# Kernel optimization log

Hardware: AMD Instinct MI355X
Metric: run time of the kernel (lower is better)

The kernel has to match this reference:

```python
import jax, jax.numpy as jnp
import numpy as np

EPS = 1e-5

def sage_layer(x, src, dst, n_tgt, Wl, bl, Wr, gamma, beta):
    # mean aggregation of source features over incoming edges per target
    msg = x[src]                                         # [E, C] irregular gather
    s = jax.ops.segment_sum(msg, dst, num_segments=n_tgt)
    cnt = jax.ops.segment_sum(jnp.ones((src.shape[0],), x.dtype), dst, num_segments=n_tgt)
    aggr = s / jnp.maximum(cnt, 1.0)[:, None]
    x_tgt = x[:n_tgt]
    h = aggr @ Wl.T + bl + x_tgt @ Wr.T                  # SAGEConv: lin_l(aggr)+lin_r(root)
    h = jax.nn.relu(h)
    mu = jnp.mean(h, axis=0)
    var = jnp.mean((h - mu) ** 2, axis=0)                # biased var (torch BN training)
    return gamma * (h - mu) * jax.lax.rsqrt(var + EPS) + beta

def setup_inputs() -> dict:
    key = jax.random.key(0)
    ks = jax.random.split(key, 16)
    C = 256
    N0, N1, N2 = 200000, 50000, 12500
    E0, E1 = 800000, 400000
    sc = 1.0 / np.sqrt(C)
    return {
        "x": jax.random.normal(ks[0], (N0, C), jnp.float32),
        "ei0_src": jax.random.randint(ks[1], (E0,), 0, N0),
        "ei0_dst": jax.random.randint(ks[2], (E0,), 0, N1),
        "ei1_src": jax.random.randint(ks[3], (E1,), 0, N1),
        "ei1_dst": jax.random.randint(ks[4], (E1,), 0, N2),
        "Wl0": jax.random.normal(ks[5], (C, C), jnp.float32) * sc,
        "bl0": jnp.zeros((C,), jnp.float32),
        "Wr0": jax.random.normal(ks[6], (C, C), jnp.float32) * sc,
        "g0": jnp.ones((C,), jnp.float32),
        "be0": jnp.zeros((C,), jnp.float32),
        "Wl1": jax.random.normal(ks[7], (C, C), jnp.float32) * sc,
        "bl1": jnp.zeros((C,), jnp.float32),
        "Wr1": jax.random.normal(ks[8], (C, C), jnp.float32) * sc,
        "g1": jnp.ones((C,), jnp.float32),
        "be1": jnp.zeros((C,), jnp.float32),
    }

def reference(x, ei0_src, ei0_dst, ei1_src, ei1_dst,
              Wl0, bl0, Wr0, g0, be0, Wl1, bl1, Wr1, g1, be1):
    N1, N2 = 50000, 12500
    x = sage_layer(x, ei0_src, ei0_dst, N1, Wl0, bl0, Wr0, g0, be0)
    x = sage_layer(x, ei1_src, ei1_dst, N2, Wl1, bl1, Wr1, g1, be1)
    return x
```

## Files before the change

kernel.cpp:

```cpp
#include <hip/hip_runtime.h>
#include <cstddef>
#include <cstdint>

#define C 256

typedef __attribute__((ext_vector_type(8))) short short8;
typedef __attribute__((ext_vector_type(4))) float f32x4;

__device__ __forceinline__ ushort f2bf(float f) {
    uint32_t u = __float_as_uint(f);
    u += 0x7FFF + ((u >> 16) & 1);
    return (ushort)(u >> 16);
}
__device__ __forceinline__ float bf2f(ushort u) {
    return __uint_as_float(((uint32_t)u) << 16);
}
__device__ __forceinline__ uint2 pack4(float a, float b, float c, float d) {
    uint2 o;
    o.x = (uint32_t)f2bf(a) | ((uint32_t)f2bf(b) << 16);
    o.y = (uint32_t)f2bf(c) | ((uint32_t)f2bf(d) << 16);
    return o;
}
__device__ __forceinline__ void acc8(uint4 v, float* a) {
    a[0] += bf2f((ushort)(v.x & 0xffff)); a[1] += bf2f((ushort)(v.x >> 16));
    a[2] += bf2f((ushort)(v.y & 0xffff)); a[3] += bf2f((ushort)(v.y >> 16));
    a[4] += bf2f((ushort)(v.z & 0xffff)); a[5] += bf2f((ushort)(v.z >> 16));
    a[6] += bf2f((ushort)(v.w & 0xffff)); a[7] += bf2f((ushort)(v.w >> 16));
}

__global__ __launch_bounds__(256) void cast_kernel(
        const float4* __restrict__ x4, int nx4, uint2* __restrict__ xbf,
        const float4* __restrict__ wl0f, const float4* __restrict__ wr0f,
        uint2* __restrict__ wl0b, uint2* __restrict__ wr0b) {
    const int nw4 = C * C / 4;
    const int total = nx4 + 2 * nw4;
    const int stride = gridDim.x * blockDim.x;
    for (int i = blockIdx.x * blockDim.x + threadIdx.x; i < total; i += stride) {
        if (i < nx4) {
            float4 v = x4[i];
            xbf[i] = pack4(v.x, v.y, v.z, v.w);
        } else if (i < nx4 + nw4) {
            int j = i - nx4;
            float4 v = wl0f[j];
            wl0b[j] = pack4(v.x, v.y, v.z, v.w);
        } else {
            int j = i - nx4 - nw4;
            float4 v = wr0f[j];
            wr0b[j] = pack4(v.x, v.y, v.z, v.w);
        }
    }
}

#define HB0 2048
#define HB1 1024
__global__ __launch_bounds__(256) void hist_kernel(
        const int* __restrict__ e0d, int* __restrict__ cnt0, int E0,
        const int* __restrict__ e1d, int* __restrict__ cnt1, int E1) {
    const int b = blockIdx.x;
    if (b < HB0) {
        const int stride = HB0 * 256;
        for (int i = b * 256 + threadIdx.x; i < E0; i += stride)
            atomicAdd(&cnt0[e0d[i]], 1);
    } else {
        const int stride = HB1 * 256;
        for (int i = (b - HB0) * 256 + threadIdx.x; i < E1; i += stride)
            atomicAdd(&cnt1[e1d[i]], 1);
    }
}

__global__ __launch_bounds__(1024) void scan2_kernel(
        const int* __restrict__ cnt0, int* __restrict__ off0, int n0,
        const int* __restrict__ cnt1, int* __restrict__ off1, int n1) {
    const int* cnt = blockIdx.x ? cnt1 : cnt0;
    int* off = blockIdx.x ? off1 : off0;
    int n = blockIdx.x ? n1 : n0;
    __shared__ int buf[1024];
    int chunk = (n + 1023) >> 10;
    int lo = (int)threadIdx.x * chunk;
    int hi = min(lo + chunk, n);
    int s = 0;
    for (int i = lo; i < hi; ++i) s += cnt[i];
    buf[threadIdx.x] = s;
    __syncthreads();
    int xv = s;
    for (int d = 1; d < 1024; d <<= 1) {
        int t = ((int)threadIdx.x >= d) ? buf[threadIdx.x - d] : 0;
        __syncthreads();
        xv += t;
        buf[threadIdx.x] = xv;
        __syncthreads();
    }
    int run = xv - s;
    for (int i = lo; i < hi; ++i) { off[i] = run; run += cnt[i]; }
    if (lo < n && hi == n) off[n] = run;
}

__global__ void scatter2_kernel(
        const int* __restrict__ s0, const int* __restrict__ d0,
        const int* __restrict__ off0, int* __restrict__ cnt0, int* __restrict__ esrc0, int E0,
        const int* __restrict__ s1, const int* __restrict__ d1,
        const int* __restrict__ off1, int* __restrict__ cnt1, int* __restrict__ esrc1, int E1) {
    int e = blockIdx.x * blockDim.x + threadIdx.x;
    if (e < E0) {
        int d = d0[e];
        int old = atomicSub(&cnt0[d], 1);
        esrc0[off0[d] + old - 1] = s0[e];
    } else if (e < E0 + E1) {
        int i = e - E0;
        int d = d1[i];
        int old = atomicSub(&cnt1[d], 1);
        esrc1[off1[d] + old - 1] = s1[i];
    }
}

__global__ __launch_bounds__(256) void aggregate_kernel(const uint4* __restrict__ xb4,
        const int* __restrict__ esrc, const int* __restrict__ off,
        uint4* __restrict__ out4, int n_tgt) {
    const int lane = threadIdx.x & 63;
    const int half = lane >> 5, l31 = lane & 31;
    const int t = blockIdx.x * 4 + (threadIdx.x >> 6);
    if (t >= n_tgt) return;
    const int base = off[t];
    const int deg = off[t + 1] - base;
    float a[8] = {0.f, 0.f, 0.f, 0.f, 0.f, 0.f, 0.f, 0.f};
    int i = 0;
    for (; i + 8 <= deg; i += 8) {
        int s0 = esrc[base + i + half];
        int s1 = esrc[base + i + 2 + half];
        int s2 = esrc[base + i + 4 + half];
        int s3 = esrc[base + i + 6 + half];
        uint4 v0 = xb4[(size_t)s0 * 32 + l31];
        uint4 v1 = xb4[(size_t)s1 * 32 + l31];
        uint4 v2 = xb4[(size_t)s2 * 32 + l31];
        uint4 v3 = xb4[(size_t)s3 * 32 + l31];
        acc8(v0, a); acc8(v1, a); acc8(v2, a); acc8(v3, a);
    }
    for (; i + 2 <= deg; i += 2) {
        int s = esrc[base + i + half];
        uint4 v = xb4[(size_t)s * 32 + l31];
        acc8(v, a);
    }
    if ((deg & 1) && half == 0) {
        int s = esrc[base + deg - 1];
        uint4 v = xb4[(size_t)s * 32 + l31];
        acc8(v, a);
    }
#pragma unroll
    for (int j = 0; j < 8; ++j) a[j] += __shfl_xor(a[j], 32, 64);
    if (half == 0) {
        float inv = 1.0f / (float)(deg > 1 ? deg : 1);
        uint4 o;
        o.x = (uint32_t)f2bf(a[0] * inv) | ((uint32_t)f2bf(a[1] * inv) << 16);
        o.y = (uint32_t)f2bf(a[2] * inv) | ((uint32_t)f2bf(a[3] * inv) << 16);
        o.z = (uint32_t)f2bf(a[4] * inv) | ((uint32_t)f2bf(a[5] * inv) << 16);
        o.w = (uint32_t)f2bf(a[6] * inv) | ((uint32_t)f2bf(a[7] * inv) << 16);
        out4[(size_t)t * 32 + l31] = o;
    }
}

__global__ __launch_bounds__(256) void aggregate_f32_kernel(const float4* __restrict__ x4,
        const int* __restrict__ esrc, const int* __restrict__ off,
        uint2* __restrict__ aggr, int n_tgt) {
    int w = threadIdx.x >> 6;
    int lane = threadIdx.x & 63;
    int t = blockIdx.x * 4 + w;
    if (t >= n_tgt) return;
    int base = off[t];
    int deg = off[t + 1] - base;
    float4 acc = make_float4(0.f, 0.f, 0.f, 0.f);
    for (int i = 0; i < deg; ++i) {
        int s = esrc[base + i];
        float4 v = x4[(size_t)s * 64 + lane];
        acc.x += v.x; acc.y += v.y; acc.z += v.z; acc.w += v.w;
    }
    float inv = 1.0f / (float)(deg > 1 ? deg : 1);
    aggr[(size_t)t * 64 + lane] = pack4(acc.x * inv, acc.y * inv, acc.z * inv, acc.w * inv);
}

#define TM 128
#define TN 128
#define LDK 40

__global__ __launch_bounds__(256) void gemm_bn_mfma(
        const ushort* __restrict__ Aagg, const ushort* __restrict__ Axt,
        const ushort* __restrict__ Wl,  const ushort* __restrict__ Wr,
        const float* __restrict__ bias,
        ushort* __restrict__ h, float* __restrict__ colsum, float* __restrict__ colsq,
        int M) {
    __shared__ ushort As[TM * LDK];
    __shared__ ushort Bs[TN * LDK];
    __shared__ float csum[TN];
    __shared__ float csq[TN];

    const int tid = threadIdx.x;
    const int m0 = blockIdx.y * TM;
    const int n0 = blockIdx.x * TN;
    const int wid = tid >> 6, lane = tid & 63;
    const int l15 = lane & 15, quad = lane >> 4;
    const int wm = (wid & 1) * 64, wn = (wid >> 1) * 64;

    if (tid < TN) { csum[tid] = 0.f; csq[tid] = 0.f; }

    const int srow = tid >> 2;
    const int skoff = (tid & 3) * 8;

    f32x4 acc[4][4];
#pragma unroll
    for (int i = 0; i < 4; ++i)
#pragma unroll
        for (int j = 0; j < 4; ++j) acc[i][j] = (f32x4){0.f, 0.f, 0.f, 0.f};

#pragma unroll 1
    for (int kt = 0; kt < 16; ++kt) {
        const int ks = kt * 32;
        const ushort* Ab = (ks < 256) ? Aagg : Axt;
        const ushort* Bb = (ks < 256) ? Wl : Wr;
        const int k0 = ks & 255;
        int r0 = min(m0 + srow, M - 1);
        int r1 = min(m0 + srow + 64, M - 1);
        uint4 a0 = *(const uint4*)&Ab[(size_t)r0 * C + k0 + skoff];
        uint4 a1 = *(const uint4*)&Ab[(size_t)r1 * C + k0 + skoff];
        uint4 b0 = *(const uint4*)&Bb[(size_t)(n0 + srow) * C + k0 + skoff];
        uint4 b1 = *(const uint4*)&Bb[(size_t)(n0 + srow + 64) * C + k0 + skoff];
        __syncthreads();
        *(uint4*)&As[srow * LDK + skoff] = a0;
        *(uint4*)&As[(srow + 64) * LDK + skoff] = a1;
        *(uint4*)&Bs[srow * LDK + skoff] = b0;
        *(uint4*)&Bs[(srow + 64) * LDK + skoff] = b1;
        __syncthreads();

        short8 af[4], bw[4];
#pragma unroll
        for (int mi = 0; mi < 4; ++mi)
            af[mi] = *(const short8*)&As[(wm + mi * 16 + l15) * LDK + quad * 8];
#pragma unroll
        for (int ni = 0; ni < 4; ++ni)
            bw[ni] = *(const short8*)&Bs[(wn + ni * 16 + l15) * LDK + quad * 8];
#pragma unroll
        for (int mi = 0; mi < 4; ++mi)
#pragma unroll
            for (int ni = 0; ni < 4; ++ni)
                acc[mi][ni] = __builtin_amdgcn_mfma_f32_16x16x32_bf16(
                    af[mi], bw[ni], acc[mi][ni], 0, 0, 0);
    }

    float lsum[4] = {0.f, 0.f, 0.f, 0.f};
    float lsq[4]  = {0.f, 0.f, 0.f, 0.f};
#pragma unroll
    for (int ni = 0; ni < 4; ++ni) {
        const int col = wn + ni * 16 + l15;
        const float bv = bias[n0 + col];
#pragma unroll
        for (int mi = 0; mi < 4; ++mi) {
#pragma unroll
            for (int r = 0; r < 4; ++r) {
                int m = m0 + wm + mi * 16 + quad * 4 + r;
                float v = acc[mi][ni][r] + bv;
                v = fmaxf(v, 0.f);
                if (m < M) {
                    h[(size_t)m * C + n0 + col] = f2bf(v);
                    lsum[ni] += v;
                    lsq[ni] += v * v;
                }
            }
        }
    }
#pragma unroll
    for (int ni = 0; ni < 4; ++ni) {
        const int col = wn + ni * 16 + l15;
        atomicAdd(&csum[col], lsum[ni]);
        atomicAdd(&csq[col], lsq[ni]);
    }
    __syncthreads();
    if (tid < TN) {
        atomicAdd(&colsum[n0 + tid], csum[tid]);
        atomicAdd(&colsq[n0 + tid], csq[tid]);
    }
}

__global__ __launch_bounds__(256) void fixup_kernel(
        const float* __restrict__ colsum, const float* __restrict__ colsq, float invN,
        const float* __restrict__ g0, const float* __restrict__ be0,
        const float* __restrict__ Wl1, const float* __restrict__ Wr1,
        const float* __restrict__ bl1,
        ushort* __restrict__ wl1b, ushort* __restrict__ wr1b, float* __restrict__ bias1) {
    __shared__ float ss[C], st[C];
    __shared__ float red[256];
    const int k = threadIdx.x;
    {
        float m = colsum[k] * invN;
        float v = colsq[k] * invN - m * m;
        float r = rsqrtf(fmaxf(v, 0.f) + 1e-5f);
        float s = g0[k] * r;
        ss[k] = s;
        st[k] = be0[k] - m * s;
    }
    __syncthreads();
    const int n = blockIdx.x;
    float wl = Wl1[(size_t)n * C + k];
    float wr = Wr1[(size_t)n * C + k];
    wl1b[(size_t)n * C + k] = f2bf(wl * ss[k]);
    wr1b[(size_t)n * C + k] = f2bf(wr * ss[k]);
    red[k] = st[k] * (wl + wr);
    __syncthreads();
    for (int d = 128; d > 0; d >>= 1) {
        if (k < d) red[k] += red[k + d];
        __syncthreads();
    }
    if (k == 0) bias1[n] = bl1[n] + red[0];
}

__global__ __launch_bounds__(256) void norm1_kernel(const uint2* __restrict__ hin,
        const float* __restrict__ colsum, const float* __restrict__ colsq, float invN,
        const float* __restrict__ gamma, const float* __restrict__ beta,
        float4* __restrict__ outp, int n4) {
    __shared__ float smu[C], srs[C];
    {
        int k = threadIdx.x;
        float m = colsum[k] * invN;
        float v = colsq[k] * invN - m * m;
        smu[k] = m;
        srs[k] = rsqrtf(fmaxf(v, 0.f) + 1e-5f);
    }
    __syncthreads();
    int i = blockIdx.x * blockDim.x + threadIdx.x;
    if (i >= n4) return;
    int c = (i & 63) << 2;
    uint2 v = hin[i];
    float4 o;
    o.x = gamma[c + 0] * (bf2f((ushort)(v.x & 0xffff)) - smu[c + 0]) * srs[c + 0] + beta[c + 0];
    o.y = gamma[c + 1] * (bf2f((ushort)(v.x >> 16))    - smu[c + 1]) * srs[c + 1] + beta[c + 1];
    o.z = gamma[c + 2] * (bf2f((ushort)(v.y & 0xffff)) - smu[c + 2]) * srs[c + 2] + beta[c + 2];
    o.w = gamma[c + 3] * (bf2f((ushort)(v.y >> 16))    - smu[c + 3]) * srs[c + 3] + beta[c + 3];
    outp[i] = o;
}

extern "C" void kernel_launch(void* const* d_in, const int* in_sizes, int n_in,
                              void* d_out, int out_size, void* d_ws, size_t ws_size,
                              hipStream_t stream) {
    const float* x   = (const float*)d_in[0];
    const int* e0s   = (const int*)d_in[1];
    const int* e0d   = (const int*)d_in[2];
    const int* e1s   = (const int*)d_in[3];
    const int* e1d   = (const int*)d_in[4];
    const float* Wl0 = (const float*)d_in[5];
    const float* bl0 = (const float*)d_in[6];
    const float* Wr0 = (const float*)d_in[7];
    const float* ga0 = (const float*)d_in[8];
    const float* be0 = (const float*)d_in[9];
    const float* Wl1 = (const float*)d_in[10];
    const float* bl1 = (const float*)d_in[11];
    const float* Wr1 = (const float*)d_in[12];
    const float* ga1 = (const float*)d_in[13];
    const float* be1 = (const float*)d_in[14];

    const int N0 = 200000, N1 = 50000, N2 = 12500;
    const int E0 = in_sizes[1];
    const int E1 = in_sizes[3];

    char* ws = (char*)d_ws;
    size_t o = 0;
    auto alloc = [&](size_t bytes) -> char* {
        char* p = ws + o;
        o += (bytes + 255) & ~(size_t)255;
        return p;
    };

    const size_t common =
        (size_t)N1 * C * 2 * 2 + (size_t)E0 * 4 + (size_t)E1 * 4 +
        ((size_t)N1 + N2 + 8 * C) * 4 + ((size_t)N1 + N2 + 2) * 4 +
        4 * (size_t)C * C * 2 + C * 4 + 65536;
    const bool full = ws_size >= common + (size_t)N0 * C * 2;

    int* cnt0 = (int*)alloc(((size_t)N1 + N2 + 8 * C) * sizeof(int));
    int* cnt1 = cnt0 + N1;
    float* stats = (float*)(cnt1 + N2);
    float* colsum0 = stats,         *colsq0 = stats + C;
    float* colsum1 = stats + 4 * C, *colsq1 = stats + 5 * C;
    const size_t zbytes = ((size_t)N1 + N2 + 8 * C) * sizeof(int);

    int* off0 = (int*)alloc(((size_t)N1 + 1) * sizeof(int));
    int* off1 = (int*)alloc(((size_t)N2 + 1) * sizeof(int));
    ushort* x_bf  = (ushort*)alloc((full ? (size_t)N0 : (size_t)N1) * C * 2);
    ushort* aggr0 = (ushort*)alloc((size_t)N1 * C * 2);
    ushort* h0raw = (ushort*)alloc((size_t)N1 * C * 2);
    ushort* aggr1 = aggr0;
    ushort* h1raw = aggr0 + (size_t)N2 * C;
    int* esrc0 = (int*)alloc((size_t)E0 * sizeof(int));
    int* esrc1 = (int*)alloc((size_t)E1 * sizeof(int));
    ushort* wbf = (ushort*)alloc(4 * (size_t)C * C * 2);
    ushort* wl0b = wbf, *wr0b = wbf + C * C, *wl1b = wbf + 2 * C * C, *wr1b = wbf + 3 * C * C;
    float* bias1 = (float*)alloc(C * sizeof(float));

    hipMemsetAsync(cnt0, 0, zbytes, stream);

    {
        int nx4 = (full ? N0 : N1) * C / 4;
        cast_kernel<<<6400, 256, 0, stream>>>((const float4*)x, nx4, (uint2*)x_bf,
                                              (const float4*)Wl0, (const float4*)Wr0,
                                              (uint2*)wl0b, (uint2*)wr0b);
    }
    hist_kernel<<<HB0 + HB1, 256, 0, stream>>>(e0d, cnt0, E0, e1d, cnt1, E1);
    scan2_kernel<<<2, 1024, 0, stream>>>(cnt0, off0, N1, cnt1, off1, N2);
    scatter2_kernel<<<(E0 + E1 + 255) / 256, 256, 0, stream>>>(
        e0s, e0d, off0, cnt0, esrc0, E0, e1s, e1d, off1, cnt1, esrc1, E1);

    if (full)
        aggregate_kernel<<<N1 / 4, 256, 0, stream>>>((const uint4*)x_bf, esrc0, off0,
                                                     (uint4*)aggr0, N1);
    else
        aggregate_f32_kernel<<<N1 / 4, 256, 0, stream>>>((const float4*)x, esrc0, off0,
                                                         (uint2*)aggr0, N1);
    dim3 grid0(C / TN, (N1 + TM - 1) / TM);
    gemm_bn_mfma<<<grid0, 256, 0, stream>>>(aggr0, x_bf, wl0b, wr0b, bl0,
                                            h0raw, colsum0, colsq0, N1);
    fixup_kernel<<<C, 256, 0, stream>>>(colsum0, colsq0, 1.0f / (float)N1,
                                        ga0, be0, Wl1, Wr1, bl1, wl1b, wr1b, bias1);

    aggregate_kernel<<<N2 / 4, 256, 0, stream>>>((const uint4*)h0raw, esrc1, off1,
                                                 (uint4*)aggr1, N2);
    dim3 grid1(C / TN, (N2 + TM - 1) / TM);
    gemm_bn_mfma<<<grid1, 256, 0, stream>>>(aggr1, h0raw, wl1b, wr1b, bias1,
                                            h1raw, colsum1, colsq1, N2);
    int n4_1 = N2 * C / 4;
    norm1_kernel<<<(n4_1 + 255) / 256, 256, 0, stream>>>((const uint2*)h1raw,
                                                         colsum1, colsq1, 1.0f / (float)N2,
                                                         ga1, be1, (float4*)d_out, n4_1);
}
```

Baseline: 697.6 us.

## Fuse whole two-layer SAGE pipeline into one cooperative persistent megakernel

Replaces the chain of separate kernels (cast, histogram, scan, scatter, aggregate, gemm, fixup, norm) with one cooperative kernel that steps through the phases separated by grid.sync. The single-block scan is replaced by a multi-block two-level scan, and the phases use grid-stride or persistent tile loops. The aim is to remove launch gaps and the serial scan bottleneck. In exchange the grid is capped at 256–512 blocks, which limits parallelism in the gather and GEMM phases, and each of the many grid barriers adds its own cost. The f32 fallback path for small workspaces is also dropped.

```diff
diff --git a/kernel.cpp b/kernel.cpp
--- a/kernel.cpp
+++ b/kernel.cpp
@@ -1,8 +1,16 @@
 #include <hip/hip_runtime.h>
+#include <hip/hip_cooperative_groups.h>
 #include <cstddef>
 #include <cstdint>
 
+namespace cg = cooperative_groups;
+
 #define C 256
+#define N1_ 50000
+#define N2_ 12500
+#define TM 128
+#define TN 128
+#define LDK 40
 
 typedef __attribute__((ext_vector_type(8))) short short8;
 typedef __attribute__((ext_vector_type(4))) float f32x4;
@@ -28,181 +36,64 @@
     a[6] += bf2f((ushort)(v.w & 0xffff)); a[7] += bf2f((ushort)(v.w >> 16));
 }
 
-__global__ __launch_bounds__(256) void cast_kernel(
-        const float4* __restrict__ x4, int nx4, uint2* __restrict__ xbf,
-        const float4* __restrict__ wl0f, const float4* __restrict__ wr0f,
-        uint2* __restrict__ wl0b, uint2* __restrict__ wr0b) {
-    const int nw4 = C * C / 4;
-    const int total = nx4 + 2 * nw4;
-    const int stride = gridDim.x * blockDim.x;
-    for (int i = blockIdx.x * blockDim.x + threadIdx.x; i < total; i += stride) {
-        if (i < nx4) {
-            float4 v = x4[i];
-            xbf[i] = pack4(v.x, v.y, v.z, v.w);
-        } else if (i < nx4 + nw4) {
-            int j = i - nx4;
-            float4 v = wl0f[j];
-            wl0b[j] = pack4(v.x, v.y, v.z, v.w);
-        } else {
-            int j = i - nx4 - nw4;
-            float4 v = wr0f[j];
-            wr0b[j] = pack4(v.x, v.y, v.z, v.w);
-        }
-    }
-}
-
-#define HB0 2048
-#define HB1 1024
-__global__ __launch_bounds__(256) void hist_kernel(
-        const int* __restrict__ e0d, int* __restrict__ cnt0, int E0,
-        const int* __restrict__ e1d, int* __restrict__ cnt1, int E1) {
-    const int b = blockIdx.x;
-    if (b < HB0) {
-        const int stride = HB0 * 256;
-        for (int i = b * 256 + threadIdx.x; i < E0; i += stride)
-            atomicAdd(&cnt0[e0d[i]], 1);
-    } else {
-        const int stride = HB1 * 256;
-        for (int i = (b - HB0) * 256 + threadIdx.x; i < E1; i += stride)
-            atomicAdd(&cnt1[e1d[i]], 1);
-    }
-}
-
-__global__ __launch_bounds__(1024) void scan2_kernel(
-        const int* __restrict__ cnt0, int* __restrict__ off0, int n0,
-        const int* __restrict__ cnt1, int* __restrict__ off1, int n1) {
-    const int* cnt = blockIdx.x ? cnt1 : cnt0;
-    int* off = blockIdx.x ? off1 : off0;
-    int n = blockIdx.x ? n1 : n0;
-    __shared__ int buf[1024];
-    int chunk = (n + 1023) >> 10;
-    int lo = (int)threadIdx.x * chunk;
-    int hi = min(lo + chunk, n);
-    int s = 0;
-    for (int i = lo; i < hi; ++i) s += cnt[i];
-    buf[threadIdx.x] = s;
+struct MegaParams {
+    const float4* x4; int nx4;
+    uint2* xbf;
+    const float4* wl0f; const float4* wr0f;
+    uint2* wl0b2; uint2* wr0b2;
+    const int* e0s; const int* e0d; int E0;
+    const int* e1s; const int* e1d; int E1;
+    int* cnt0; int* cnt1;
+    int* off0; int* off1;
+    int* bsum0; int* bbase0; int* bsum1; int* bbase1;
+    int* esrc0; int* esrc1;
+    const ushort* xbf_u;
+    ushort* aggr0; ushort* h0raw; ushort* aggr1; ushort* h1raw;
+    const ushort* wl0b; const ushort* wr0b;
+    ushort* wl1b; ushort* wr1b;
+    const float* bl0; const float* ga0; const float* be0;
+    const float* Wl1f; const float* Wr1f; const float* bl1;
+    float* bias1;
+    const float* ga1; const float* be1;
+    float* colsum0; float* colsq0; float* colsum1; float* colsq1;
+    float4* out;
+};
+
+union alignas(16) Smem {
+    int scan[256];
+    struct { ushort As[TM * LDK]; ushort Bs[TN * LDK]; float csum[TN]; float csq[TN]; } g;
+    struct { float ss[C]; float st[C]; float red[256]; } fx;
+    struct { float mu[C]; float rs[C]; } nm;
+};
+
+__device__ __forceinline__ int block_incl_scan(int v, int* buf) {
+    const int t = threadIdx.x;
+    buf[t] = v;
     __syncthreads();
-    int xv = s;
-    for (int d = 1; d < 1024; d <<= 1) {
-        int t = ((int)threadIdx.x >= d) ? buf[threadIdx.x - d] : 0;
-        __syncthreads();
-        xv += t;
-        buf[threadIdx.x] = xv;
-        __syncthreads();
-    }
-    int run = xv - s;
-    for (int i = lo; i < hi; ++i) { off[i] = run; run += cnt[i]; }
-    if (lo < n && hi == n) off[n] = run;
-}
-
-__global__ void scatter2_kernel(
-        const int* __restrict__ s0, const int* __restrict__ d0,
-        const int* __restrict__ off0, int* __restrict__ cnt0, int* __restrict__ esrc0, int E0,
-        const int* __restrict__ s1, const int* __restrict__ d1,
-        const int* __restrict__ off1, int* __restrict__ cnt1, int* __restrict__ esrc1, int E1) {
-    int e = blockIdx.x * blockDim.x + threadIdx.x;
-    if (e < E0) {
-        int d = d0[e];
-        int old = atomicSub(&cnt0[d], 1);
-        esrc0[off0[d] + old - 1] = s0[e];
-    } else if (e < E0 + E1) {
-        int i = e - E0;
-        int d = d1[i];
-        int old = atomicSub(&cnt1[d], 1);
-        esrc1[off1[d] + old - 1] = s1[i];
-    }
-}
-
-__global__ __launch_bounds__(256) void aggregate_kernel(const uint4* __restrict__ xb4,
-        const int* __restrict__ esrc, const int* __restrict__ off,
-        uint4* __restrict__ out4, int n_tgt) {
-    const int lane = threadIdx.x & 63;
-    const int half = lane >> 5, l31 = lane & 31;
-    const int t = blockIdx.x * 4 + (threadIdx.x >> 6);
-    if (t >= n_tgt) return;
-    const int base = off[t];
-    const int deg = off[t + 1] - base;
-    float a[8] = {0.f, 0.f, 0.f, 0.f, 0.f, 0.f, 0.f, 0.f};
-    int i = 0;
-    for (; i + 8 <= deg; i += 8) {
-        int s0 = esrc[base + i + half];
-        int s1 = esrc[base + i + 2 + half];
-        int s2 = esrc[base + i + 4 + half];
-        int s3 = esrc[base + i + 6 + half];
-        uint4 v0 = xb4[(size_t)s0 * 32 + l31];
-        uint4 v1 = xb4[(size_t)s1 * 32 + l31];
-        uint4 v2 = xb4[(size_t)s2 * 32 + l31];
-        uint4 v3 = xb4[(size_t)s3 * 32 + l31];
-        acc8(v0, a); acc8(v1, a); acc8(v2, a); acc8(v3, a);
-    }
-    for (; i + 2 <= deg; i += 2) {
-        int s = esrc[base + i + half];
-        uint4 v = xb4[(size_t)s * 32 + l31];
-        acc8(v, a);
-    }
-    if ((deg & 1) && half == 0) {
-        int s = esrc[base + deg - 1];
-        uint4 v = xb4[(size_t)s * 32 + l31];
-        acc8(v, a);
-    }
-#pragma unroll
-    for (int j = 0; j < 8; ++j) a[j] += __shfl_xor(a[j], 32, 64);
-    if (half == 0) {
-        float inv = 1.0f / (float)(deg > 1 ? deg : 1);
-        uint4 o;
-        o.x = (uint32_t)f2bf(a[0] * inv) | ((uint32_t)f2bf(a[1] * inv) << 16);
-        o.y = (uint32_t)f2bf(a[2] * inv) | ((uint32_t)f2bf(a[3] * inv) << 16);
-        o.z = (uint32_t)f2bf(a[4] * inv) | ((uint32_t)f2bf(a[5] * inv) << 16);
-        o.w = (uint32_t)f2bf(a[6] * inv) | ((uint32_t)f2bf(a[7] * inv) << 16);
-        out4[(size_t)t * 32 + l31] = o;
-    }
-}
-
-__global__ __launch_bounds__(256) void aggregate_f32_kernel(const float4* __restrict__ x4,
-        const int* __restrict__ esrc, const int* __restrict__ off,
-        uint2* __restrict__ aggr, int n_tgt) {
-    int w = threadIdx.x >> 6;
-    int lane = threadIdx.x & 63;
-    int t = blockIdx.x * 4 + w;
-    if (t >= n_tgt) return;
-    int base = off[t];
-    int deg = off[t + 1] - base;
-    float4 acc = make_float4(0.f, 0.f, 0.f, 0.f);
-    for (int i = 0; i < deg; ++i) {
-        int s = esrc[base + i];
-        float4 v = x4[(size_t)s * 64 + lane];
-        acc.x += v.x; acc.y += v.y; acc.z += v.z; acc.w += v.w;
-    }
-    float inv = 1.0f / (float)(deg > 1 ? deg : 1);
-    aggr[(size_t)t * 64 + lane] = pack4(acc.x * inv, acc.y * inv, acc.z * inv, acc.w * inv);
-}
-
-#define TM 128
-#define TN 128
-#define LDK 40
-
-__global__ __launch_bounds__(256) void gemm_bn_mfma(
-        const ushort* __restrict__ Aagg, const ushort* __restrict__ Axt,
-        const ushort* __restrict__ Wl,  const ushort* __restrict__ Wr,
-        const float* __restrict__ bias,
-        ushort* __restrict__ h, float* __restrict__ colsum, float* __restrict__ colsq,
-        int M) {
-    __shared__ ushort As[TM * LDK];
-    __shared__ ushort Bs[TN * LDK];
-    __shared__ float csum[TN];
-    __shared__ float csq[TN];
-
+    for (int d = 1; d < 256; d <<= 1) {
+        int o = (t >= d) ? buf[t - d] : 0;
+        __syncthreads();
+        buf[t] += o;
+        __syncthreads();
+    }
+    return buf[t];
+}
+
+__device__ void gemm_tile(int tile, const ushort* __restrict__ Aagg, const ushort* __restrict__ Axt,
+                          const ushort* __restrict__ Wl, const ushort* __restrict__ Wr,
+                          const float* __restrict__ bias, ushort* __restrict__ h,
+                          float* __restrict__ colsum, float* __restrict__ colsq,
+                          int M, Smem& sm) {
     const int tid = threadIdx.x;
-    const int m0 = blockIdx.y * TM;
-    const int n0 = blockIdx.x * TN;
+    const int n0 = (tile & 1) * TN;
+    const int m0 = (tile >> 1) * TM;
     const int wid = tid >> 6, lane = tid & 63;
     const int l15 = lane & 15, quad = lane >> 4;
     const int wm = (wid & 1) * 64, wn = (wid >> 1) * 64;
-
-    if (tid < TN) { csum[tid] = 0.f; csq[tid] = 0.f; }
-
     const int srow = tid >> 2;
     const int skoff = (tid & 3) * 8;
+
+    if (tid < TN) { sm.g.csum[tid] = 0.f; sm.g.csq[tid] = 0.f; }
 
     f32x4 acc[4][4];
 #pragma unroll
@@ -223,19 +114,19 @@
         uint4 b0 = *(const uint4*)&Bb[(size_t)(n0 + srow) * C + k0 + skoff];
         uint4 b1 = *(const uint4*)&Bb[(size_t)(n0 + srow + 64) * C + k0 + skoff];
         __syncthreads();
-        *(uint4*)&As[srow * LDK + skoff] = a0;
-        *(uint4*)&As[(srow + 64) * LDK + skoff] = a1;
-        *(uint4*)&Bs[srow * LDK + skoff] = b0;
-        *(uint4*)&Bs[(srow + 64) * LDK + skoff] = b1;
+        *(uint4*)&sm.g.As[srow * LDK + skoff] = a0;
+        *(uint4*)&sm.g.As[(srow + 64) * LDK + skoff] = a1;
+        *(uint4*)&sm.g.Bs[srow * LDK + skoff] = b0;
+        *(uint4*)&sm.g.Bs[(srow + 64) * LDK + skoff] = b1;
         __syncthreads();
 
         short8 af[4], bw[4];
 #pragma unroll
         for (int mi = 0; mi < 4; ++mi)
-            af[mi] = *(const short8*)&As[(wm + mi * 16 + l15) * LDK + quad * 8];
+            af[mi] = *(const short8*)&sm.g.As[(wm + mi * 16 + l15) * LDK + quad * 8];
 #pragma unroll
         for (int ni = 0; ni < 4; ++ni)
-            bw[ni] = *(const short8*)&Bs[(wn + ni * 16 + l15) * LDK + quad * 8];
+            bw[ni] = *(const short8*)&sm.g.Bs[(wn + ni * 16 + l15) * LDK + quad * 8];
 #pragma unroll
         for (int mi = 0; mi < 4; ++mi)
 #pragma unroll
@@ -268,71 +159,217 @@
 #pragma unroll
     for (int ni = 0; ni < 4; ++ni) {
         const int col = wn + ni * 16 + l15;
-        atomicAdd(&csum[col], lsum[ni]);
-        atomicAdd(&csq[col], lsq[ni]);
+        atomicAdd(&sm.g.csum[col], lsum[ni]);
+        atomicAdd(&sm.g.csq[col], lsq[ni]);
     }
     __syncthreads();
     if (tid < TN) {
-        atomicAdd(&colsum[n0 + tid], csum[tid]);
-        atomicAdd(&colsq[n0 + tid], csq[tid]);
-    }
-}
-
-__global__ __launch_bounds__(256) void fixup_kernel(
-        const float* __restrict__ colsum, const float* __restrict__ colsq, float invN,
-        const float* __restrict__ g0, const float* __restrict__ be0,
-        const float* __restrict__ Wl1, const float* __restrict__ Wr1,
-        const float* __restrict__ bl1,
-        ushort* __restrict__ wl1b, ushort* __restrict__ wr1b, float* __restrict__ bias1) {
-    __shared__ float ss[C], st[C];
-    __shared__ float red[256];
-    const int k = threadIdx.x;
-    {
-        float m = colsum[k] * invN;
-        float v = colsq[k] * invN - m * m;
+        atomicAdd(&colsum[n0 + tid], sm.g.csum[tid]);
+        atomicAdd(&colsq[n0 + tid], sm.g.csq[tid]);
+    }
+}
+
+__device__ void aggregate_phase(const uint4* __restrict__ xb4, const int* __restrict__ esrc,
+                                const int* __restrict__ off, uint4* __restrict__ out4,
+                                int n_tgt, int nwaves) {
+    const int tid = threadIdx.x;
+    const int lane = tid & 63;
+    const int half = lane >> 5, l31 = lane & 31;
+    const int gw = blockIdx.x * 4 + (tid >> 6);
+    for (int t = gw; t < n_tgt; t += nwaves) {
+        const int base = off[t];
+        const int deg = off[t + 1] - base;
+        float a[8] = {0.f, 0.f, 0.f, 0.f, 0.f, 0.f, 0.f, 0.f};
+        int i = 0;
+        for (; i + 8 <= deg; i += 8) {
+            int s0 = esrc[base + i + half];
+            int s1 = esrc[base + i + 2 + half];
+            int s2 = esrc[base + i + 4 + half];
+            int s3 = esrc[base + i + 6 + half];
+            uint4 v0 = xb4[(size_t)s0 * 32 + l31];
+            uint4 v1 = xb4[(size_t)s1 * 32 + l31];
+            uint4 v2 = xb4[(size_t)s2 * 32 + l31];
+            uint4 v3 = xb4[(size_t)s3 * 32 + l31];
+            acc8(v0, a); acc8(v1, a); acc8(v2, a); acc8(v3, a);
+        }
+        for (; i + 2 <= deg; i += 2) {
+            int s = esrc[base + i + half];
+            uint4 v = xb4[(size_t)s * 32 + l31];
+            acc8(v, a);
+        }
+        if ((deg & 1) && half == 0) {
+            int s = esrc[base + deg - 1];
+            uint4 v = xb4[(size_t)s * 32 + l31];
+            acc8(v, a);
+        }
+#pragma unroll
+        for (int j = 0; j < 8; ++j) a[j] += __shfl_xor(a[j], 32, 64);
+        if (half == 0) {
+            float inv = 1.0f / (float)(deg > 1 ? deg : 1);
+            uint4 o;
+            o.x = (uint32_t)f2bf(a[0] * inv) | ((uint32_t)f2bf(a[1] * inv) << 16);
+            o.y = (uint32_t)f2bf(a[2] * inv) | ((uint32_t)f2bf(a[3] * inv) << 16);
+            o.z = (uint32_t)f2bf(a[4] * inv) | ((uint32_t)f2bf(a[5] * inv) << 16);
+            o.w = (uint32_t)f2bf(a[6] * inv) | ((uint32_t)f2bf(a[7] * inv) << 16);
+            out4[(size_t)t * 32 + l31] = o;
+        }
+    }
+}
+
+__global__ __launch_bounds__(256, 2) void mega_kernel(MegaParams p) {
+    cg::grid_group grid = cg::this_grid();
+    __shared__ Smem sm;
+    const int tid = threadIdx.x;
+    const int nblk = gridDim.x;
+    const int gtid = blockIdx.x * 256 + tid;
+    const int gsz = nblk * 256;
+    const int nwaves = nblk * 4;
+
+    {
+        const int nw4 = C * C / 4;
+        const int total = p.nx4 + 2 * nw4;
+        for (int i = gtid; i < total; i += gsz) {
+            if (i < p.nx4) {
+                float4 v = p.x4[i];
+                p.xbf[i] = pack4(v.x, v.y, v.z, v.w);
+            } else if (i < p.nx4 + nw4) {
+                int j = i - p.nx4;
+                float4 v = p.wl0f[j];
+                p.wl0b2[j] = pack4(v.x, v.y, v.z, v.w);
+            } else {
+                int j = i - p.nx4 - nw4;
+                float4 v = p.wr0f[j];
+                p.wr0b2[j] = pack4(v.x, v.y, v.z, v.w);
+            }
+        }
+        for (int i = gtid; i < p.E0; i += gsz) atomicAdd(&p.cnt0[p.e0d[i]], 1);
+        for (int i = gtid; i < p.E1; i += gsz) atomicAdd(&p.cnt1[p.e1d[i]], 1);
+    }
+    __threadfence(); grid.sync();
+
+    const int ch0 = (N1_ + nblk - 1) / nblk;
+    const int ch1 = (N2_ + nblk - 1) / nblk;
+    {
+        int i0 = blockIdx.x * ch0 + tid;
+        int v0 = (tid < ch0 && i0 < N1_) ? p.cnt0[i0] : 0;
+        int incl0 = block_incl_scan(v0, sm.scan);
+        if (tid == 255) p.bsum0[blockIdx.x] = incl0;
+        __syncthreads();
+        int i1 = blockIdx.x * ch1 + tid;
+        int v1 = (tid < ch1 && i1 < N2_) ? p.cnt1[i1] : 0;
+        int incl1 = block_incl_scan(v1, sm.scan);
+        if (tid == 255) p.bsum1[blockIdx.x] = incl1;
+    }
+    __threadfence(); grid.sync();
+
+    if (blockIdx.x < 2) {
+        const int* bs = blockIdx.x ? p.bsum1 : p.bsum0;
+        int* bb = blockIdx.x ? p.bbase1 : p.bbase0;
+        int a0 = (2 * tid < nblk) ? bs[2 * tid] : 0;
+        int a1 = (2 * tid + 1 < nblk) ? bs[2 * tid + 1] : 0;
+        int s = a0 + a1;
+        int incl = block_incl_scan(s, sm.scan);
+        int excl = incl - s;
+        if (2 * tid < nblk) bb[2 * tid] = excl;
+        if (2 * tid + 1 < nblk) bb[2 * tid + 1] = excl + a0;
+        if (tid == 255) {
+            if (blockIdx.x) p.off1[N2_] = incl;
+            else p.off0[N1_] = incl;
+        }
+    }
+    __threadfence(); grid.sync();
+
+    {
+        int i0 = blockIdx.x * ch0 + tid;
+        int v0 = (tid < ch0 && i0 < N1_) ? p.cnt0[i0] : 0;
+        int incl0 = block_incl_scan(v0, sm.scan);
+        if (tid < ch0 && i0 < N1_) p.off0[i0] = p.bbase0[blockIdx.x] + incl0 - v0;
+        __syncthreads();
+        int i1 = blockIdx.x * ch1 + tid;
+        int v1 = (tid < ch1 && i1 < N2_) ? p.cnt1[i1] : 0;
+        int incl1 = block_incl_scan(v1, sm.scan);
+        if (tid < ch1 && i1 < N2_) p.off1[i1] = p.bbase1[blockIdx.x] + incl1 - v1;
+    }
+    __threadfence(); grid.sync();
+
+    {
+        for (int e = gtid; e < p.E0; e += gsz) {
+            int d = p.e0d[e];
+            int old = atomicSub(&p.cnt0[d], 1);
+            p.esrc0[p.off0[d] + old - 1] = p.e0s[e];
+        }
+        for (int e = gtid; e < p.E1; e += gsz) {
+            int d = p.e1d[e];
+            int old = atomicSub(&p.cnt1[d], 1);
+            p.esrc1[p.off1[d] + old - 1] = p.e1s[e];
+        }
+    }
+    __threadfence(); grid.sync();
+
+    aggregate_phase((const uint4*)p.xbf_u, p.esrc0, p.off0, (uint4*)p.aggr0, N1_, nwaves);
+    __threadfence(); grid.sync();
+
+    {
+        const int ntiles = ((N1_ + TM - 1) / TM) * 2;
+        for (int t = blockIdx.x; t < ntiles; t += nblk)
+            gemm_tile(t, p.aggr0, p.xbf_u, p.wl0b, p.wr0b, p.bl0,
+                      p.h0raw, p.colsum0, p.colsq0, N1_, sm);
+    }
+    __threadfence(); grid.sync();
+
+    if (blockIdx.x < 256) {
+        const float invN = 1.0f / (float)N1_;
+        float m = p.colsum0[tid] * invN;
+        float v = p.colsq0[tid] * invN - m * m;
         float r = rsqrtf(fmaxf(v, 0.f) + 1e-5f);
-        float s = g0[k] * r;
-        ss[k] = s;
-        st[k] = be0[k] - m * s;
-    }
-    __syncthreads();
-    const int n = blockIdx.x;
-    float wl = Wl1[(size_t)n * C + k];
-    float wr = Wr1[(size_t)n * C + k];
-    wl1b[(size_t)n * C + k] = f2bf(wl * ss[k]);
-    wr1b[(size_t)n * C + k] = f2bf(wr * ss[k]);
-    red[k] = st[k] * (wl + wr);
-    __syncthreads();
-    for (int d = 128; d > 0; d >>= 1) {
-        if (k < d) red[k] += red[k + d];
-        __syncthreads();
-    }
-    if (k == 0) bias1[n] = bl1[n] + red[0];
-}
-
-__global__ __launch_bounds__(256) void norm1_kernel(const uint2* __restrict__ hin,
-        const float* __restrict__ colsum, const float* __restrict__ colsq, float invN,
-        const float* __restrict__ gamma, const float* __restrict__ beta,
-        float4* __restrict__ outp, int n4) {
-    __shared__ float smu[C], srs[C];
-    {
-        int k = threadIdx.x;
-        float m = colsum[k] * invN;
-        float v = colsq[k] * invN - m * m;
-        smu[k] = m;
-        srs[k] = rsqrtf(fmaxf(v, 0.f) + 1e-5f);
-    }
-    __syncthreads();
-    int i = blockIdx.x * blockDim.x + threadIdx.x;
-    if (i >= n4) return;
-    int c = (i & 63) << 2;
-    uint2 v = hin[i];
-    float4 o;
-    o.x = gamma[c + 0] * (bf2f((ushort)(v.x & 0xffff)) - smu[c + 0]) * srs[c + 0] + beta[c + 0];
-    o.y = gamma[c + 1] * (bf2f((ushort)(v.x >> 16))    - smu[c + 1]) * srs[c + 1] + beta[c + 1];
-    o.z = gamma[c + 2] * (bf2f((ushort)(v.y & 0xffff)) - smu[c + 2]) * srs[c + 2] + beta[c + 2];
-    o.w = gamma[c + 3] * (bf2f((ushort)(v.y >> 16))    - smu[c + 3]) * srs[c + 3] + beta[c + 3];
-    outp[i] = o;
+        float s = p.ga0[tid] * r;
+        sm.fx.ss[tid] = s;
+        sm.fx.st[tid] = p.be0[tid] - m * s;
+        __syncthreads();
+        const int n = blockIdx.x;
+        float wl = p.Wl1f[(size_t)n * C + tid];
+        float wr = p.Wr1f[(size_t)n * C + tid];
+        p.wl1b[(size_t)n * C + tid] = f2bf(wl * sm.fx.ss[tid]);
+        p.wr1b[(size_t)n * C + tid] = f2bf(wr * sm.fx.ss[tid]);
+        sm.fx.red[tid] = sm.fx.st[tid] * (wl + wr);
+        __syncthreads();
+        for (int d = 128; d > 0; d >>= 1) {
+            if (tid < d) sm.fx.red[tid] += sm.fx.red[tid + d];
+            __syncthreads();
+        }
+        if (tid == 0) p.bias1[n] = p.bl1[n] + sm.fx.red[0];
+    }
+    aggregate_phase((const uint4*)p.h0raw, p.esrc1, p.off1, (uint4*)p.aggr1, N2_, nwaves);
+    __threadfence(); grid.sync();
+
+    {
+        const int ntiles = ((N2_ + TM - 1) / TM) * 2;
+        for (int t = blockIdx.x; t < ntiles; t += nblk)
+            gemm_tile(t, p.aggr1, p.h0raw, p.wl1b, p.wr1b, p.bias1,
+                      p.h1raw, p.colsum1, p.colsq1, N2_, sm);
+    }
+    __threadfence(); grid.sync();
+
+    {
+        const float invN = 1.0f / (float)N2_;
+        float m = p.colsum1[tid] * invN;
+        float v = p.colsq1[tid] * invN - m * m;
+        sm.nm.mu[tid] = p.ga1[tid] * rsqrtf(fmaxf(v, 0.f) + 1e-5f);
+        sm.nm.rs[tid] = p.be1[tid] - m * sm.nm.mu[tid];
+        __syncthreads();
+        const uint2* hin = (const uint2*)p.h1raw;
+        const int n4 = N2_ * C / 4;
+        for (int i = gtid; i < n4; i += gsz) {
+            int c = (i & 63) << 2;
+            uint2 v2 = hin[i];
+            float4 o;
+            o.x = bf2f((ushort)(v2.x & 0xffff)) * sm.nm.mu[c + 0] + sm.nm.rs[c + 0];
+            o.y = bf2f((ushort)(v2.x >> 16))    * sm.nm.mu[c + 1] + sm.nm.rs[c + 1];
+            o.z = bf2f((ushort)(v2.y & 0xffff)) * sm.nm.mu[c + 2] + sm.nm.rs[c + 2];
+            o.w = bf2f((ushort)(v2.y >> 16))    * sm.nm.mu[c + 3] + sm.nm.rs[c + 3];
+            p.out[i] = o;
+        }
+    }
 }
 
 extern "C" void kernel_launch(void* const* d_in, const int* in_sizes, int n_in,
@@ -354,7 +391,7 @@
     const float* ga1 = (const float*)d_in[13];
     const float* be1 = (const float*)d_in[14];
 
-    const int N0 = 200000, N1 = 50000, N2 = 12500;
+    const int N0 = 200000;
     const int E0 = in_sizes[1];
     const int E1 = in_sizes[3];
 
@@ -366,26 +403,24 @@
         return p;
     };
 
-    const size_t common =
-        (size_t)N1 * C * 2 * 2 + (size_t)E0 * 4 + (size_t)E1 * 4 +
-        ((size_t)N1 + N2 + 8 * C) * 4 + ((size_t)N1 + N2 + 2) * 4 +
-        4 * (size_t)C * C * 2 + C * 4 + 65536;
-    const bool full = ws_size >= common + (size_t)N0 * C * 2;
-
-    int* cnt0 = (int*)alloc(((size_t)N1 + N2 + 8 * C) * sizeof(int));
-    int* cnt1 = cnt0 + N1;
-    float* stats = (float*)(cnt1 + N2);
+    int* cnt0 = (int*)alloc(((size_t)N1_ + N2_ + 8 * C) * sizeof(int));
+    int* cnt1 = cnt0 + N1_;
+    float* stats = (float*)(cnt1 + N2_);
     float* colsum0 = stats,         *colsq0 = stats + C;
     float* colsum1 = stats + 4 * C, *colsq1 = stats + 5 * C;
-    const size_t zbytes = ((size_t)N1 + N2 + 8 * C) * sizeof(int);
-
-    int* off0 = (int*)alloc(((size_t)N1 + 1) * sizeof(int));
-    int* off1 = (int*)alloc(((size_t)N2 + 1) * sizeof(int));
-    ushort* x_bf  = (ushort*)alloc((full ? (size_t)N0 : (size_t)N1) * C * 2);
-    ushort* aggr0 = (ushort*)alloc((size_t)N1 * C * 2);
-    ushort* h0raw = (ushort*)alloc((size_t)N1 * C * 2);
+    const size_t zbytes = ((size_t)N1_ + N2_ + 8 * C) * sizeof(int);
+
+    int* off0 = (int*)alloc(((size_t)N1_ + 1) * sizeof(int));
+    int* off1 = (int*)alloc(((size_t)N2_ + 1) * sizeof(int));
+    int* bsum0  = (int*)alloc(512 * sizeof(int));
+    int* bbase0 = (int*)alloc(512 * sizeof(int));
+    int* bsum1  = (int*)alloc(512 * sizeof(int));
+    int* bbase1 = (int*)alloc(512 * sizeof(int));
+    ushort* x_bf  = (ushort*)alloc((size_t)N0 * C * 2);
+    ushort* aggr0 = (ushort*)alloc((size_t)N1_ * C * 2);
+    ushort* h0raw = (ushort*)alloc((size_t)N1_ * C * 2);
     ushort* aggr1 = aggr0;
-    ushort* h1raw = aggr0 + (size_t)N2 * C;
+    ushort* h1raw = aggr0 + (size_t)N2_ * C;
     int* esrc0 = (int*)alloc((size_t)E0 * sizeof(int));
     int* esrc1 = (int*)alloc((size_t)E1 * sizeof(int));
     ushort* wbf = (ushort*)alloc(4 * (size_t)C * C * 2);
@@ -394,36 +429,36 @@
 
     hipMemsetAsync(cnt0, 0, zbytes, stream);
 
-    {
-        int nx4 = (full ? N0 : N1) * C / 4;
-        cast_kernel<<<6400, 256, 0, stream>>>((const float4*)x, nx4, (uint2*)x_bf,
-                                              (const float4*)Wl0, (const float4*)Wr0,
-                                              (uint2*)wl0b, (uint2*)wr0b);
-    }
-    hist_kernel<<<HB0 + HB1, 256, 0, stream>>>(e0d, cnt0, E0, e1d, cnt1, E1);
-    scan2_kernel<<<2, 1024, 0, stream>>>(cnt0, off0, N1, cnt1, off1, N2);
-    scatter2_kernel<<<(E0 + E1 + 255) / 256, 256, 0, stream>>>(
-        e0s, e0d, off0, cnt0, esrc0, E0, e1s, e1d, off1, cnt1, esrc1, E1);
-
-    if (full)
-        aggregate_kernel<<<N1 / 4, 256, 0, stream>>>((const uint4*)x_bf, esrc0, off0,
-                                                     (uint4*)aggr0, N1);
-    else
-        aggregate_f32_kernel<<<N1 / 4, 256, 0, stream>>>((const float4*)x, esrc0, off0,
-                                                         (uint2*)aggr0, N1);
-    dim3 grid0(C / TN, (N1 + TM - 1) / TM);
-    gemm_bn_mfma<<<grid0, 256, 0, stream>>>(aggr0, x_bf, wl0b, wr0b, bl0,
-                                            h0raw, colsum0, colsq0, N1);
-    fixup_kernel<<<C, 256, 0, stream>>>(colsum0, colsq0, 1.0f / (float)N1,
-                                        ga0, be0, Wl1, Wr1, bl1, wl1b, wr1b, bias1);
-
-    aggregate_kernel<<<N2 / 4, 256, 0, stream>>>((const uint4*)h0raw, esrc1, off1,
-                                                 (uint4*)aggr1, N2);
-    dim3 grid1(C / TN, (N2 + TM - 1) / TM);
-    gemm_bn_mfma<<<grid1, 256, 0, stream>>>(aggr1, h0raw, wl1b, wr1b, bias1,
-                                            h1raw, colsum1, colsq1, N2);
-    int n4_1 = N2 * C / 4;
-    norm1_kernel<<<(n4_1 + 255) / 256, 256, 0, stream>>>((const uint2*)h1raw,
-                                                         colsum1, colsq1, 1.0f / (float)N2,
-                                                         ga1, be1, (float4*)d_out, n4_1);
-}
+    int occ = 0;
+    hipError_t oe = hipOccupancyMaxActiveBlocksPerMultiprocessor(&occ, (const void*)mega_kernel, 256, 0);
+    if (oe != hipSuccess || occ < 1) occ = 1;
+    int nblk = occ * 256;
+    if (nblk > 512) nblk = 512;
+    if (nblk < 256) nblk = 256;
+
+    MegaParams p;
+    p.x4 = (const float4*)x; p.nx4 = N0 * C / 4;
+    p.xbf = (uint2*)x_bf;
+    p.wl0f = (const float4*)Wl0; p.wr0f = (const float4*)Wr0;
+    p.wl0b2 = (uint2*)wl0b; p.wr0b2 = (uint2*)wr0b;
+    p.e0s = e0s; p.e0d = e0d; p.E0 = E0;
+    p.e1s = e1s; p.e1d = e1d; p.E1 = E1;
+    p.cnt0 = cnt0; p.cnt1 = cnt1;
+    p.off0 = off0; p.off1 = off1;
+    p.bsum0 = bsum0; p.bbase0 = bbase0; p.bsum1 = bsum1; p.bbase1 = bbase1;
+    p.esrc0 = esrc0; p.esrc1 = esrc1;
+    p.xbf_u = x_bf;
+    p.aggr0 = aggr0; p.h0raw = h0raw; p.aggr1 = aggr1; p.h1raw = h1raw;
+    p.wl0b = wl0b; p.wr0b = wr0b;
+    p.wl1b = wl1b; p.wr1b = wr1b;
+    p.bl0 = bl0; p.ga0 = ga0; p.be0 = be0;
+    p.Wl1f = Wl1; p.Wr1f = Wr1; p.bl1 = bl1;
+    p.bias1 = bias1;
+    p.ga1 = ga1; p.be1 = be1;
+    p.colsum0 = colsum0; p.colsq0 = colsq0; p.colsum1 = colsum1; p.colsq1 = colsq1;
+    p.out = (float4*)d_out;
+
+    void* args[] = { &p };
+    hipLaunchCooperativeKernel((const void*)mega_kernel, dim3(nblk), dim3(256),
+                               args, 0, stream);
+}
```

Result: slower. 1.298 ms (+86.0%).
